# Kernel optimization log

Hardware: AMD Instinct MI355X
Metric: run time of the kernel (lower is better)

Reference implementation:

```python
import jax, jax.numpy as jnp
import numpy as np

N = 4096          # in_features
M = 4096          # out_features
RANK = 64
FT = 16           # ft_rank (trainable LoRA)
RES = RANK - FT   # frozen low-rank residual
CB = 65536        # E8P: 16-bit codeword per group of 8 weights
CW = 8            # codeword width (E8 lattice dim)
Q_SCALE = 0.02
GLOBAL_SCALE = 1.0


def _hadamard(n):
    # Sylvester construction, normalized: H @ H.T = I (matches matmul_hadU/hadUt up to transpose; H is symmetric)
    H = np.array([[1.0]], dtype=np.float32)
    while H.shape[0] < n:
        H = np.block([[H, H], [H, -H]])
    return H / np.sqrt(np.float32(n))


def setup_inputs() -> dict:
    key = jax.random.key(0)
    ks = jax.random.split(key, 9)
    x = jax.random.normal(ks[0], (8192, N), jnp.float32)
    Q_idxs = jax.random.randint(ks[1], (M, N // CW), 0, CB, dtype=jnp.int32)
    grid = jax.random.normal(ks[2], (CB, CW), jnp.float32) * 0.5   # E8P codebook grid
    SU = jax.random.rademacher(ks[3], (N,), dtype=jnp.float32)     # random sign vectors (QuIP#)
    SV = jax.random.rademacher(ks[4], (M,), dtype=jnp.float32)
    L_ft = jax.random.normal(ks[5], (M, FT), jnp.float32) * 0.02
    R_ft = jax.random.normal(ks[6], (FT, N), jnp.float32) * 0.02
    L_res = jax.random.normal(ks[7], (M, RES), jnp.float32) * 0.02
    R_res = jax.random.normal(ks[8], (RES, N), jnp.float32) * 0.02
    had_left = jnp.asarray(_hadamard(N))
    had_right = jnp.asarray(_hadamard(M))
    return {"x": x, "SU": SU, "SV": SV, "grid": grid, "L_ft": L_ft, "R_ft": R_ft,
            "L_res": L_res, "R_res": R_res, "had_left": had_left,
            "had_right": had_right, "Q_idxs": Q_idxs}


def reference(x, SU, SV, grid, L_ft, R_ft, L_res, R_res, had_left, had_right, Q_idxs):
    shape = x.shape
    h = x.reshape(-1, N) * SU                 # x * SU
    h = h @ had_left                          # matmul_hadUt (Hadamard is symmetric orthogonal)
    # E8P codebook decode: gather 8-dim codewords -> full [M, N] weight, fused matmul
    W = grid[Q_idxs].reshape(M, N)            # [M, N//8, 8] -> [M, N]
    out = (h @ W.T) * Q_SCALE                 # Q.forward
    out = out + (h @ R_res.T) @ L_res.T       # frozen low-rank residual (rank - ft_rank)
    out = out + (h @ R_ft.T) @ L_ft.T         # trainable LoRA path
    out = (out @ had_right) * GLOBAL_SCALE    # matmul_hadU * global_scale
    out = out * SV
    return out.reshape(*shape[:-1], M)
```

## Files before the change

### kernel.cpp

```cpp
#include <hip/hip_runtime.h>
#include <hip/hip_bf16.h>
#include <stdint.h>


typedef __bf16 bf16;
typedef __bf16 bf16x8 __attribute__((ext_vector_type(8)));
typedef float f32x4 __attribute__((ext_vector_type(4)));

#define KE 4160
#define KT_MAIN 130
#define NN 4096
#define MM 4096
#define BB 8192

__global__ void prep_kernel(const float* __restrict__ Lft, const float* __restrict__ Rft,
                            const float* __restrict__ Lres, const float* __restrict__ Rres,
                            bf16* __restrict__ Rcat, bf16* __restrict__ Wq) {
  int tid = blockIdx.x * 256 + threadIdx.x;
  if (tid < 64 * 4096) {
    int r = tid >> 12, n = tid & 4095;
    float v = (r < 48) ? Rres[r * 4096 + n] : Rft[(r - 48) * 4096 + n];
    Rcat[tid] = (bf16)v;
  } else {
    int t2 = tid - 64 * 4096;
    int m = t2 >> 6, r = t2 & 63;
    float v = (r < 48) ? Lres[m * 48 + r] : Lft[m * 16 + (r - 48)];
    Wq[(size_t)m * KE + 4096 + r] = (bf16)v;
  }
}

__global__ void decode_kernel(const int* __restrict__ qidx, const float* __restrict__ grid,
                              bf16* __restrict__ Wq) {
  int tid = blockIdx.x * 256 + threadIdx.x;
  int m = tid >> 9, g = tid & 511;
  uint32_t idx = (uint32_t)qidx[tid];
  const float4* gp = (const float4*)(grid + (size_t)idx * 8);
  float4 w0 = gp[0], w1 = gp[1];
  bf16x8 o;
  o[0] = (bf16)(w0.x * 0.02f); o[1] = (bf16)(w0.y * 0.02f);
  o[2] = (bf16)(w0.z * 0.02f); o[3] = (bf16)(w0.w * 0.02f);
  o[4] = (bf16)(w1.x * 0.02f); o[5] = (bf16)(w1.y * 0.02f);
  o[6] = (bf16)(w1.z * 0.02f); o[7] = (bf16)(w1.w * 0.02f);
  *(bf16x8*)(Wq + (size_t)m * KE + g * 8) = o;
}

__global__ void fwht_pre_kernel(const float* __restrict__ src,
                                bf16* __restrict__ dst,
                                const float* __restrict__ SU) {
  __shared__ float buf[4096];
  const int row = blockIdx.x, t = threadIdx.x;
  const float4* sp = (const float4*)(src + (size_t)row * NN + t * 16);
  const float4* su = (const float4*)(SU + t * 16);
  float v[16];
#pragma unroll
  for (int q = 0; q < 4; ++q) {
    float4 a = sp[q], s = su[q];
    v[q * 4 + 0] = a.x * s.x; v[q * 4 + 1] = a.y * s.y;
    v[q * 4 + 2] = a.z * s.z; v[q * 4 + 3] = a.w * s.w;
  }
#pragma unroll
  for (int s = 1; s < 16; s <<= 1) {
#pragma unroll
    for (int i = 0; i < 16; ++i) {
      if (!(i & s)) { float a = v[i], b = v[i + s]; v[i] = a + b; v[i + s] = a - b; }
    }
  }
#pragma unroll
  for (int i = 0; i < 16; ++i) buf[t * 16 + i] = v[i];
  for (int s = 16; s < 4096; s <<= 1) {
    __syncthreads();
#pragma unroll
    for (int j = 0; j < 8; ++j) {
      int p = t + j * 256;
      int i = ((p & ~(s - 1)) << 1) | (p & (s - 1));
      float a = buf[i], b = buf[i + s];
      buf[i] = a + b; buf[i + s] = a - b;
    }
  }
  __syncthreads();
  bf16x8 o0, o1;
#pragma unroll
  for (int i = 0; i < 8; ++i) {
    o0[i] = (bf16)(buf[t * 16 + i] * 0.015625f);
    o1[i] = (bf16)(buf[t * 16 + 8 + i] * 0.015625f);
  }
  bf16* dp = dst + (size_t)row * KE + t * 16;
  *(bf16x8*)dp = o0;
  *(bf16x8*)(dp + 8) = o1;
}

__global__ void fwht_post_kernel(float* __restrict__ data, const float* __restrict__ SV) {
  __shared__ float buf[4096];
  const int row = blockIdx.x, t = threadIdx.x;
  float4* dp = (float4*)(data + (size_t)row * MM + t * 16);
  float v[16];
#pragma unroll
  for (int q = 0; q < 4; ++q) {
    float4 a = dp[q];
    v[q * 4 + 0] = a.x; v[q * 4 + 1] = a.y; v[q * 4 + 2] = a.z; v[q * 4 + 3] = a.w;
  }
#pragma unroll
  for (int s = 1; s < 16; s <<= 1) {
#pragma unroll
    for (int i = 0; i < 16; ++i) {
      if (!(i & s)) { float a = v[i], b = v[i + s]; v[i] = a + b; v[i + s] = a - b; }
    }
  }
#pragma unroll
  for (int i = 0; i < 16; ++i) buf[t * 16 + i] = v[i];
  for (int s = 16; s < 4096; s <<= 1) {
    __syncthreads();
#pragma unroll
    for (int j = 0; j < 8; ++j) {
      int p = t + j * 256;
      int i = ((p & ~(s - 1)) << 1) | (p & (s - 1));
      float a = buf[i], b = buf[i + s];
      buf[i] = a + b; buf[i + s] = a - b;
    }
  }
  __syncthreads();
  const float4* sv = (const float4*)(SV + t * 16);
#pragma unroll
  for (int q = 0; q < 4; ++q) {
    float4 s = sv[q];
    float4 o;
    o.x = buf[t * 16 + q * 4 + 0] * 0.015625f * s.x;
    o.y = buf[t * 16 + q * 4 + 1] * 0.015625f * s.y;
    o.z = buf[t * 16 + q * 4 + 2] * 0.015625f * s.z;
    o.w = buf[t * 16 + q * 4 + 3] * 0.015625f * s.w;
    dp[q] = o;
  }
}

__global__ void __launch_bounds__(256) tgemm_kernel(const bf16* __restrict__ A,
                                                    const bf16* __restrict__ Bm,
                                                    float* __restrict__ Tpart) {
  __shared__ bf16 lA[128 * 32];
  __shared__ bf16 lB[64 * 32];
  const int t = threadIdx.x, w = t >> 6, l = t & 63;
  const int bmBlk = blockIdx.x;
  const int split = blockIdx.y;
  const int wm = w >> 1, wn = w & 1;
  f32x4 acc[4][2] = {};
  const int arow = t >> 1, acol = (t & 1) * 16;
  const bf16* pa = A + (size_t)(bmBlk * 128 + arow) * KE + acol;
  const int brow = (t & 127) >> 1, bcol = acol;
  const bf16* pb = Bm + (size_t)brow * 4096 + bcol;
  const int fr = l & 15, fk = (l >> 4) * 8;
  for (int kt = 0; kt < 32; ++kt) {
    const int k0 = (split * 32 + kt) * 32;
    bf16x8 a0 = *(const bf16x8*)(pa + k0);
    bf16x8 a1 = *(const bf16x8*)(pa + k0 + 8);
    *(bf16x8*)&lA[arow * 32 + acol] = a0;
    *(bf16x8*)&lA[arow * 32 + acol + 8] = a1;
    if (t < 128) {
      bf16x8 b0 = *(const bf16x8*)(pb + k0);
      bf16x8 b1 = *(const bf16x8*)(pb + k0 + 8);
      *(bf16x8*)&lB[brow * 32 + bcol] = b0;
      *(bf16x8*)&lB[brow * 32 + bcol + 8] = b1;
    }
    __syncthreads();
    bf16x8 af[4], bfr[2];
#pragma unroll
    for (int i = 0; i < 4; ++i) af[i] = *(const bf16x8*)&lA[(wm * 64 + i * 16 + fr) * 32 + fk];
#pragma unroll
    for (int i = 0; i < 2; ++i) bfr[i] = *(const bf16x8*)&lB[(wn * 32 + i * 16 + fr) * 32 + fk];
#pragma unroll
    for (int mi = 0; mi < 4; ++mi)
#pragma unroll
      for (int ni = 0; ni < 2; ++ni)
        acc[mi][ni] = __builtin_amdgcn_mfma_f32_16x16x32_bf16(af[mi], bfr[ni], acc[mi][ni], 0, 0, 0);
    __syncthreads();
  }
  float* out = Tpart + (size_t)split * BB * 64;
  const int orow = bmBlk * 128 + wm * 64 + (l >> 4) * 4;
  const int ocol = wn * 32 + (l & 15);
#pragma unroll
  for (int mi = 0; mi < 4; ++mi)
#pragma unroll
    for (int ni = 0; ni < 2; ++ni)
#pragma unroll
      for (int r = 0; r < 4; ++r)
        out[(size_t)(orow + mi * 16 + r) * 64 + ocol + ni * 16] = acc[mi][ni][r];
}

__global__ void tconv_kernel(const float* __restrict__ Tpart, bf16* __restrict__ h) {
  int i = blockIdx.x * 256 + threadIdx.x;
  float s = Tpart[i] + Tpart[i + BB * 64] + Tpart[i + 2 * BB * 64] + Tpart[i + 3 * BB * 64];
  int row = i >> 6, c = i & 63;
  h[(size_t)row * KE + 4096 + c] = (bf16)s;
}

__global__ void __launch_bounds__(256) mgemm_kernel(const bf16* __restrict__ A,
                                                    const bf16* __restrict__ B,
                                                    float* __restrict__ C) {
  __shared__ bf16 lA[128 * 32];
  __shared__ bf16 lB[128 * 32];
  const int t = threadIdx.x, w = t >> 6, l = t & 63;
  const int bn = blockIdx.x, bm = blockIdx.y;
  const int wm = w >> 1, wn = w & 1;
  f32x4 acc[4][4] = {};
  const int srow = t >> 1, scol = (t & 1) * 16;
  const bf16* pa = A + (size_t)(bm * 128 + srow) * KE + scol;
  const bf16* pb = B + (size_t)(bn * 128 + srow) * KE + scol;
  const int fr = l & 15, fk = (l >> 4) * 8;
  for (int kt = 0; kt < KT_MAIN; ++kt) {
    const int k0 = kt * 32;
    bf16x8 a0 = *(const bf16x8*)(pa + k0);
    bf16x8 a1 = *(const bf16x8*)(pa + k0 + 8);
    bf16x8 b0 = *(const bf16x8*)(pb + k0);
    bf16x8 b1 = *(const bf16x8*)(pb + k0 + 8);
    *(bf16x8*)&lA[srow * 32 + scol] = a0;
    *(bf16x8*)&lA[srow * 32 + scol + 8] = a1;
    *(bf16x8*)&lB[srow * 32 + scol] = b0;
    *(bf16x8*)&lB[srow * 32 + scol + 8] = b1;
    __syncthreads();
    bf16x8 af[4], bfr[4];
#pragma unroll
    for (int i = 0; i < 4; ++i) {
      af[i] = *(const bf16x8*)&lA[(wm * 64 + i * 16 + fr) * 32 + fk];
      bfr[i] = *(const bf16x8*)&lB[(wn * 64 + i * 16 + fr) * 32 + fk];
    }
#pragma unroll
    for (int mi = 0; mi < 4; ++mi)
#pragma unroll
      for (int ni = 0; ni < 4; ++ni)
        acc[mi][ni] = __builtin_amdgcn_mfma_f32_16x16x32_bf16(af[mi], bfr[ni], acc[mi][ni], 0, 0, 0);
    __syncthreads();
  }
  const int orow = bm * 128 + wm * 64 + (l >> 4) * 4;
  const int ocol = bn * 128 + wn * 64 + (l & 15);
#pragma unroll
  for (int mi = 0; mi < 4; ++mi)
#pragma unroll
    for (int ni = 0; ni < 4; ++ni)
#pragma unroll
      for (int r = 0; r < 4; ++r)
        C[(size_t)(orow + mi * 16 + r) * MM + ocol + ni * 16] = acc[mi][ni][r];
}

extern "C" void kernel_launch(void* const* d_in, const int* in_sizes, int n_in,
                              void* d_out, int out_size, void* d_ws, size_t ws_size,
                              hipStream_t stream) {
  const float* x    = (const float*)d_in[0];
  const float* SU   = (const float*)d_in[1];
  const float* SV   = (const float*)d_in[2];
  const float* grid = (const float*)d_in[3];
  const float* Lft  = (const float*)d_in[4];
  const float* Rft  = (const float*)d_in[5];
  const float* Lres = (const float*)d_in[6];
  const float* Rres = (const float*)d_in[7];
  const int*   qidx = (const int*)d_in[10];
  float* out = (float*)d_out;

  char* ws = (char*)d_ws;
  bf16*  h     = (bf16*)ws;
  bf16*  Wq    = (bf16*)(ws + 68157440);
  bf16*  Rcat  = (bf16*)(ws + 68157440 + 34078720);
  float* Tpart = (float*)(ws + 68157440 + 34078720 + 524288);

  prep_kernel<<<2048, 256, 0, stream>>>(Lft, Rft, Lres, Rres, Rcat, Wq);
  decode_kernel<<<8192, 256, 0, stream>>>(qidx, grid, Wq);
  fwht_pre_kernel<<<8192, 256, 0, stream>>>(x, h, SU);
  tgemm_kernel<<<dim3(64, 4), 256, 0, stream>>>(h, Rcat, Tpart);
  tconv_kernel<<<2048, 256, 0, stream>>>(Tpart, h);
  mgemm_kernel<<<dim3(32, 64), 256, 0, stream>>>(h, Wq, out);
  fwht_post_kernel<<<8192, 256, 0, stream>>>(out, SV);
}
```

Measured before the change: 752.1 us.

## Rewrite main GEMM with 256x256 tiles, direct-to-LDS multistage pipeline, and padded FWHT LDS

```diff
diff --git a/kernel.cpp b/kernel.cpp
--- a/kernel.cpp
+++ b/kernel.cpp
@@ -8,7 +8,6 @@
 typedef float f32x4 __attribute__((ext_vector_type(4)));
 
 #define KE 4160
-#define KT_MAIN 130
 #define NN 4096
 #define MM 4096
 #define BB 8192
@@ -44,10 +43,12 @@
   *(bf16x8*)(Wq + (size_t)m * KE + g * 8) = o;
 }
 
+#define SK(i) ((i) + ((i) >> 5))
+
 __global__ void fwht_pre_kernel(const float* __restrict__ src,
                                 bf16* __restrict__ dst,
                                 const float* __restrict__ SU) {
-  __shared__ float buf[4096];
+  __shared__ float buf[4224];
   const int row = blockIdx.x, t = threadIdx.x;
   const float4* sp = (const float4*)(src + (size_t)row * NN + t * 16);
   const float4* su = (const float4*)(SU + t * 16);
@@ -66,23 +67,23 @@
     }
   }
 #pragma unroll
-  for (int i = 0; i < 16; ++i) buf[t * 16 + i] = v[i];
+  for (int i = 0; i < 16; ++i) buf[SK(t * 16 + i)] = v[i];
   for (int s = 16; s < 4096; s <<= 1) {
     __syncthreads();
 #pragma unroll
     for (int j = 0; j < 8; ++j) {
       int p = t + j * 256;
       int i = ((p & ~(s - 1)) << 1) | (p & (s - 1));
-      float a = buf[i], b = buf[i + s];
-      buf[i] = a + b; buf[i + s] = a - b;
+      float a = buf[SK(i)], b = buf[SK(i + s)];
+      buf[SK(i)] = a + b; buf[SK(i + s)] = a - b;
     }
   }
   __syncthreads();
   bf16x8 o0, o1;
 #pragma unroll
   for (int i = 0; i < 8; ++i) {
-    o0[i] = (bf16)(buf[t * 16 + i] * 0.015625f);
-    o1[i] = (bf16)(buf[t * 16 + 8 + i] * 0.015625f);
+    o0[i] = (bf16)(buf[SK(t * 16 + i)] * 0.015625f);
+    o1[i] = (bf16)(buf[SK(t * 16 + 8 + i)] * 0.015625f);
   }
   bf16* dp = dst + (size_t)row * KE + t * 16;
   *(bf16x8*)dp = o0;
@@ -90,7 +91,7 @@
 }
 
 __global__ void fwht_post_kernel(float* __restrict__ data, const float* __restrict__ SV) {
-  __shared__ float buf[4096];
+  __shared__ float buf[4224];
   const int row = blockIdx.x, t = threadIdx.x;
   float4* dp = (float4*)(data + (size_t)row * MM + t * 16);
   float v[16];
@@ -107,15 +108,15 @@
     }
   }
 #pragma unroll
-  for (int i = 0; i < 16; ++i) buf[t * 16 + i] = v[i];
+  for (int i = 0; i < 16; ++i) buf[SK(t * 16 + i)] = v[i];
   for (int s = 16; s < 4096; s <<= 1) {
     __syncthreads();
 #pragma unroll
     for (int j = 0; j < 8; ++j) {
       int p = t + j * 256;
       int i = ((p & ~(s - 1)) << 1) | (p & (s - 1));
-      float a = buf[i], b = buf[i + s];
-      buf[i] = a + b; buf[i + s] = a - b;
+      float a = buf[SK(i)], b = buf[SK(i + s)];
+      buf[SK(i)] = a + b; buf[SK(i + s)] = a - b;
     }
   }
   __syncthreads();
@@ -124,10 +125,10 @@
   for (int q = 0; q < 4; ++q) {
     float4 s = sv[q];
     float4 o;
-    o.x = buf[t * 16 + q * 4 + 0] * 0.015625f * s.x;
-    o.y = buf[t * 16 + q * 4 + 1] * 0.015625f * s.y;
-    o.z = buf[t * 16 + q * 4 + 2] * 0.015625f * s.z;
-    o.w = buf[t * 16 + q * 4 + 3] * 0.015625f * s.w;
+    o.x = buf[SK(t * 16 + q * 4 + 0)] * 0.015625f * s.x;
+    o.y = buf[SK(t * 16 + q * 4 + 1)] * 0.015625f * s.y;
+    o.z = buf[SK(t * 16 + q * 4 + 2)] * 0.015625f * s.z;
+    o.w = buf[SK(t * 16 + q * 4 + 3)] * 0.015625f * s.w;
     dp[q] = o;
   }
 }
@@ -191,47 +192,118 @@
   h[(size_t)row * KE + 4096 + c] = (bf16)s;
 }
 
-__global__ void __launch_bounds__(256) mgemm_kernel(const bf16* __restrict__ A,
-                                                    const bf16* __restrict__ B,
-                                                    float* __restrict__ C) {
-  __shared__ bf16 lA[128 * 32];
-  __shared__ bf16 lB[128 * 32];
-  const int t = threadIdx.x, w = t >> 6, l = t & 63;
-  const int bn = blockIdx.x, bm = blockIdx.y;
-  const int wm = w >> 1, wn = w & 1;
-  f32x4 acc[4][4] = {};
-  const int srow = t >> 1, scol = (t & 1) * 16;
-  const bf16* pa = A + (size_t)(bm * 128 + srow) * KE + scol;
-  const bf16* pb = B + (size_t)(bn * 128 + srow) * KE + scol;
-  const int fr = l & 15, fk = (l >> 4) * 8;
-  for (int kt = 0; kt < KT_MAIN; ++kt) {
-    const int k0 = kt * 32;
-    bf16x8 a0 = *(const bf16x8*)(pa + k0);
-    bf16x8 a1 = *(const bf16x8*)(pa + k0 + 8);
-    bf16x8 b0 = *(const bf16x8*)(pb + k0);
-    bf16x8 b1 = *(const bf16x8*)(pb + k0 + 8);
-    *(bf16x8*)&lA[srow * 32 + scol] = a0;
-    *(bf16x8*)&lA[srow * 32 + scol + 8] = a1;
-    *(bf16x8*)&lB[srow * 32 + scol] = b0;
-    *(bf16x8*)&lB[srow * 32 + scol + 8] = b1;
-    __syncthreads();
-    bf16x8 af[4], bfr[4];
-#pragma unroll
-    for (int i = 0; i < 4; ++i) {
-      af[i] = *(const bf16x8*)&lA[(wm * 64 + i * 16 + fr) * 32 + fk];
-      bfr[i] = *(const bf16x8*)&lB[(wn * 64 + i * 16 + fr) * 32 + fk];
-    }
+
+__device__ __forceinline__ void gload16(const void* g, void* l) {
+  __builtin_amdgcn_global_load_lds(
+      (const __attribute__((address_space(1))) void*)g,
+      (__attribute__((address_space(3))) void*)l, 16, 0, 0);
+}
+
+__device__ __forceinline__ void bar() {
+  asm volatile("" ::: "memory");
+  __builtin_amdgcn_s_barrier();
+  asm volatile("" ::: "memory");
+}
+
+__global__ void __launch_bounds__(512, 2) mgemm_kernel(const bf16* __restrict__ A,
+                                                       const bf16* __restrict__ B,
+                                                       float* __restrict__ C) {
+  __shared__ alignas(16) char sA[65536];
+  __shared__ alignas(16) char sB[65536];
+  const int t = threadIdx.x;
+  const int w = t >> 6, l = t & 63;
+  const int wm = w >> 2, wn = w & 3;
+  const int bid = blockIdx.x;
+  const int swzb = (bid & 7) * 64 + (bid >> 3);
+  const int bm = swzb >> 4, bn = swzb & 15;
+
+  const int c0 = w * 2, c1 = w * 2 + 1;
+  const int lb0 = c0 * 1024 + l * 16;
+  const int lb1 = c1 * 1024 + l * 16;
+  const int sb0 = lb0 ^ (((lb0 >> 7) & 3) << 4);
+  const int sb1 = lb1 ^ (((lb1 >> 7) & 3) << 4);
+  const char* gA0 = (const char*)(A + (size_t)(bm * 256 + (sb0 >> 6)) * KE) + (sb0 & 63);
+  const char* gA1 = (const char*)(A + (size_t)(bm * 256 + (sb1 >> 6)) * KE) + (sb1 & 63);
+  const char* gB0 = (const char*)(B + (size_t)(bn * 256 + (sb0 >> 6)) * KE) + (sb0 & 63);
+  const char* gB1 = (const char*)(B + (size_t)(bn * 256 + (sb1 >> 6)) * KE) + (sb1 & 63);
+
+  const int fr = l & 15, fkb = (l >> 4) * 16;
+  int offA[8], offB[4];
+#pragma unroll
+  for (int mi = 0; mi < 8; ++mi) {
+    int lb = (wm * 128 + mi * 16 + fr) * 64 + fkb;
+    offA[mi] = lb ^ (((lb >> 7) & 3) << 4);
+  }
+#pragma unroll
+  for (int ni = 0; ni < 4; ++ni) {
+    int lb = (wn * 64 + ni * 16 + fr) * 64 + fkb;
+    offB[ni] = lb ^ (((lb >> 7) & 3) << 4);
+  }
+
+  f32x4 acc[8][4] = {};
+
+#pragma unroll
+  for (int p = 0; p < 3; ++p) {
+    gload16(gA0 + (size_t)p * 64, &sA[p * 16384 + c0 * 1024]);
+    gload16(gA1 + (size_t)p * 64, &sA[p * 16384 + c1 * 1024]);
+    gload16(gB0 + (size_t)p * 64, &sB[p * 16384 + c0 * 1024]);
+    gload16(gB1 + (size_t)p * 64, &sB[p * 16384 + c1 * 1024]);
+  }
+  asm volatile("s_waitcnt vmcnt(8)" ::: "memory");
+  __builtin_amdgcn_sched_barrier(0);
+  bar();
+
+  for (int i = 0; i < 130; ++i) {
+    const int sbs = (i & 3) << 14;
+    const int s3b = ((i + 3) & 3) << 14;
+    const size_t ko = (size_t)(i + 3) << 6;
+    bf16x8 af[4], bv[4];
+#pragma unroll
+    for (int mi = 0; mi < 4; ++mi) af[mi] = *(const bf16x8*)&sA[sbs + offA[mi]];
+#pragma unroll
+    for (int ni = 0; ni < 4; ++ni) bv[ni] = *(const bf16x8*)&sB[sbs + offB[ni]];
+    if (i < 127) {
+      gload16(gA0 + ko, &sA[s3b + c0 * 1024]);
+      gload16(gA1 + ko, &sA[s3b + c1 * 1024]);
+    }
+    bar();
+    __builtin_amdgcn_s_setprio(1);
 #pragma unroll
     for (int mi = 0; mi < 4; ++mi)
 #pragma unroll
       for (int ni = 0; ni < 4; ++ni)
-        acc[mi][ni] = __builtin_amdgcn_mfma_f32_16x16x32_bf16(af[mi], bfr[ni], acc[mi][ni], 0, 0, 0);
-    __syncthreads();
-  }
-  const int orow = bm * 128 + wm * 64 + (l >> 4) * 4;
-  const int ocol = bn * 128 + wn * 64 + (l & 15);
-#pragma unroll
-  for (int mi = 0; mi < 4; ++mi)
+        acc[mi][ni] = __builtin_amdgcn_mfma_f32_16x16x32_bf16(af[mi], bv[ni], acc[mi][ni], 0, 0, 0);
+    __builtin_amdgcn_s_setprio(0);
+    bar();
+#pragma unroll
+    for (int mi = 0; mi < 4; ++mi) af[mi] = *(const bf16x8*)&sA[sbs + offA[4 + mi]];
+    if (i < 127) {
+      gload16(gB0 + ko, &sB[s3b + c0 * 1024]);
+      gload16(gB1 + ko, &sB[s3b + c1 * 1024]);
+      asm volatile("s_waitcnt vmcnt(8)" ::: "memory");
+      __builtin_amdgcn_sched_barrier(0);
+    } else if (i == 127) {
+      asm volatile("s_waitcnt vmcnt(4)" ::: "memory");
+      __builtin_amdgcn_sched_barrier(0);
+    } else if (i == 128) {
+      asm volatile("s_waitcnt vmcnt(0)" ::: "memory");
+      __builtin_amdgcn_sched_barrier(0);
+    }
+    bar();
+    __builtin_amdgcn_s_setprio(1);
+#pragma unroll
+    for (int mi = 0; mi < 4; ++mi)
+#pragma unroll
+      for (int ni = 0; ni < 4; ++ni)
+        acc[4 + mi][ni] = __builtin_amdgcn_mfma_f32_16x16x32_bf16(af[mi], bv[ni], acc[4 + mi][ni], 0, 0, 0);
+    __builtin_amdgcn_s_setprio(0);
+    bar();
+  }
+
+  const int orow = bm * 256 + wm * 128 + ((l >> 4) << 2);
+  const int ocol = bn * 256 + wn * 64 + (l & 15);
+#pragma unroll
+  for (int mi = 0; mi < 8; ++mi)
 #pragma unroll
     for (int ni = 0; ni < 4; ++ni)
 #pragma unroll
@@ -264,6 +336,6 @@
   fwht_pre_kernel<<<8192, 256, 0, stream>>>(x, h, SU);
   tgemm_kernel<<<dim3(64, 4), 256, 0, stream>>>(h, Rcat, Tpart);
   tconv_kernel<<<2048, 256, 0, stream>>>(Tpart, h);
-  mgemm_kernel<<<dim3(32, 64), 256, 0, stream>>>(h, Wq, out);
+  mgemm_kernel<<<512, 512, 0, stream>>>(h, Wq, out);
   fwht_post_kernel<<<8192, 256, 0, stream>>>(out, SV);
 }
```

Result: faster. 647.6 us (-13.9%).
